# Kernel optimization log

Measured on AMD Instinct MI355X. Metric: run time of the kernel, lower is better.

## Reference

```python
import jax, jax.numpy as jnp
import numpy as np


def setup_inputs() -> dict:
    B, D, H, O = 16, 128, 2048, 4
    W = O * H + O  # 8196 flattened last-layer params
    ks = jax.random.split(jax.random.key(0), 6)
    return {
        "x": jax.random.normal(ks[0], (B, D), dtype=jnp.float32),
        "W1": jax.random.normal(ks[1], (H, D), dtype=jnp.float32) * 0.05,
        "b1": jax.random.normal(ks[2], (H,), dtype=jnp.float32) * 0.01,
        "W2": jax.random.normal(ks[3], (O, H), dtype=jnp.float32) * 0.02,
        "b2": jax.random.normal(ks[4], (O,), dtype=jnp.float32) * 0.01,
        "inv_covariance": jax.random.normal(ks[5], (W, W), dtype=jnp.float32) * 0.01,
    }


def reference(x, W1, b1, W2, b2, inv_covariance):
    # Wrapped model: MLP with ReLU; uncertainty layer = last Linear(H->O).
    O, H = W2.shape
    h = jax.nn.relu(x @ W1.T + b1)          # [B, H] penultimate activations
    predictions = h @ W2.T + b2             # [B, O]

    # Jacobian of each output element w.r.t. flattened last-layer params
    # (weight then bias), matching torch's per-output autograd.grad loop but
    # vectorized: vmap over batch of jacrev over the parameter vector.
    p0 = jnp.concatenate([W2.reshape(-1), b2])  # [W]

    def head(p, h_b):
        w2 = p[: O * H].reshape(O, H)
        b = p[O * H :]
        return h_b @ w2.T + b               # [O]

    J = jax.vmap(lambda h_b: jax.jacrev(head)(p0, h_b))(h)  # [B, O, W]

    # uncertainty = diag of per-(b,o) quadratic form J Sigma^{-1} J^T
    uncertainty = jnp.einsum('bow,wv,bov->bo', J, inv_covariance, J)
    return predictions, uncertainty
```

## Files before the change

kernel.cpp:

```cpp
#include <hip/hip_runtime.h>

#define BB 16
#define DD 128
#define HH 2048
#define OO 4
#define WTOT 8196
#define OHH 8192
#define KC 32
#define NQUAD 512
#define NCROSS 32


__global__ __launch_bounds__(256) void k_prep(const float* __restrict__ x,
                                              const float* __restrict__ W1,
                                              const float* __restrict__ b1,
                                              float* __restrict__ hT) {
    __shared__ float xs[DD * BB];
    int tid = threadIdx.x;
    for (int i = tid; i < DD * BB; i += 256) {
        int b = i & 15, d = i >> 4;
        xs[i] = x[b * DD + d];
    }
    __syncthreads();
    int b = tid & 15;
    int j = blockIdx.x * 16 + (tid >> 4);
    const float4* W1v = (const float4*)(W1 + (size_t)j * DD);
    float acc = 0.0f;
#pragma unroll
    for (int dd = 0; dd < DD / 4; ++dd) {
        float4 w = W1v[dd];
        acc = fmaf(xs[(dd * 4 + 0) * 16 + b], w.x, acc);
        acc = fmaf(xs[(dd * 4 + 1) * 16 + b], w.y, acc);
        acc = fmaf(xs[(dd * 4 + 2) * 16 + b], w.z, acc);
        acc = fmaf(xs[(dd * 4 + 3) * 16 + b], w.w, acc);
    }
    acc += b1[j];
    hT[j * 16 + b] = acc > 0.0f ? acc : 0.0f;
}

__global__ __launch_bounds__(256) void k_main(const float* __restrict__ C,
                                              const float* __restrict__ hT,
                                              const float* __restrict__ W2,
                                              float* __restrict__ qpart,
                                              float* __restrict__ xu,
                                              float* __restrict__ xp) {
    int bid = blockIdx.x;
    int tid = threadIdx.x;
    __shared__ float sh[KC * 16];
    __shared__ float red[4 * 16];

    if (bid < NQUAD) {
        int o  = bid & 3;
        int ct = (bid >> 2) & 1;
        int kc = bid >> 3;
        if (tid < KC * 16 / 4)
            ((float4*)sh)[tid] = ((const float4*)(hT + (size_t)kc * KC * 16))[tid];
        __syncthreads();

        int base = o * HH;
        const float4* Cp = (const float4*)(C + (size_t)(base + kc * KC) * WTOT
                                             + base + ct * 1024) + tid;
        float acc[16][4];
#pragma unroll
        for (int b = 0; b < 16; ++b)
#pragma unroll
            for (int c = 0; c < 4; ++c) acc[b][c] = 0.0f;

#pragma unroll 4
        for (int k = 0; k < KC; ++k) {
            float4 c4 = Cp[(size_t)k * (WTOT / 4)];
#pragma unroll
            for (int b = 0; b < 16; ++b) {
                float hb = sh[k * 16 + b];
                acc[b][0] = fmaf(hb, c4.x, acc[b][0]);
                acc[b][1] = fmaf(hb, c4.y, acc[b][1]);
                acc[b][2] = fmaf(hb, c4.z, acc[b][2]);
                acc[b][3] = fmaf(hb, c4.w, acc[b][3]);
            }
        }

        int col0 = ct * 1024 + 4 * tid;
        float v[16];
#pragma unroll
        for (int b = 0; b < 16; ++b) v[b] = 0.0f;
#pragma unroll
        for (int c = 0; c < 4; ++c) {
            const float* hc = hT + (size_t)(col0 + c) * 16;
#pragma unroll
            for (int b = 0; b < 16; ++b)
                v[b] = fmaf(acc[b][c], hc[b], v[b]);
        }

#pragma unroll
        for (int b = 0; b < 16; ++b) {
            float s = v[b];
#pragma unroll
            for (int off = 32; off > 0; off >>= 1)
                s += __shfl_down(s, off, 64);
            v[b] = s;
        }
        int lane = tid & 63, wv = tid >> 6;
        if (lane == 0) {
#pragma unroll
            for (int b = 0; b < 16; ++b) red[wv * 16 + b] = v[b];
        }
        __syncthreads();
        if (tid < 16)
            qpart[bid * 16 + tid] = red[tid] + red[16 + tid] + red[32 + tid] + red[48 + tid];
    } else {
        int cb = bid - NQUAD;
        int o  = cb & 3;
        int kb = cb >> 2;
        int b = tid >> 4, g = tid & 15;
        int base = o * HH;
        float a12 = 0.0f, ap = 0.0f;
#pragma unroll 4
        for (int i = 0; i < 16; ++i) {
            int k = kb * 256 + i * 16 + g;
            float hv = hT[k * 16 + b];
            float c1 = C[(size_t)(base + k) * WTOT + OHH + o];
            float c2 = C[(size_t)(OHH + o) * WTOT + base + k];
            float w2 = W2[o * HH + k];
            a12 = fmaf(hv, c1 + c2, a12);
            ap  = fmaf(hv, w2, ap);
        }
#pragma unroll
        for (int off = 8; off > 0; off >>= 1) {
            a12 += __shfl_down(a12, off, 16);
            ap  += __shfl_down(ap, off, 16);
        }
        if (g == 0) {
            xu[cb * 16 + b] = a12;
            xp[cb * 16 + b] = ap;
        }
    }
}

__global__ void k_final(const float* __restrict__ C,
                        const float* __restrict__ qpart,
                        const float* __restrict__ xu,
                        const float* __restrict__ xp,
                        const float* __restrict__ b2,
                        float* __restrict__ out) {
    int i = threadIdx.x;
    int b = i >> 2, o = i & 3;
    float u = 0.0f, p = 0.0f;
    for (int q = o; q < NQUAD; q += 4) u += qpart[q * 16 + b];
    for (int c = o; c < NCROSS; c += 4) {
        u += xu[c * 16 + b];
        p += xp[c * 16 + b];
    }
    out[i] = p + b2[o];
    out[64 + i] = u + C[(size_t)(OHH + o) * WTOT + OHH + o];
}

extern "C" void kernel_launch(void* const* d_in, const int* in_sizes, int n_in,
                              void* d_out, int out_size, void* d_ws, size_t ws_size,
                              hipStream_t stream) {
    const float* x  = (const float*)d_in[0];
    const float* W1 = (const float*)d_in[1];
    const float* b1 = (const float*)d_in[2];
    const float* W2 = (const float*)d_in[3];
    const float* b2 = (const float*)d_in[4];
    const float* C  = (const float*)d_in[5];
    float* out = (float*)d_out;

    float* hT    = (float*)d_ws;
    float* qpart = hT + HH * BB;
    float* xu    = qpart + NQUAD * 16;
    float* xp    = xu + NCROSS * 16;

    hipLaunchKernelGGL(k_prep,  dim3(HH / 16),        dim3(256), 0, stream, x, W1, b1, hT);
    hipLaunchKernelGGL(k_main,  dim3(NQUAD + NCROSS), dim3(256), 0, stream, C, hT, W2, qpart, xu, xp);
    hipLaunchKernelGGL(k_final, dim3(1),              dim3(64),  0, stream, C, qpart, xu, xp, b2, out);
}
```

Measured before the change: 362.2 us.

## Double-buffer C tiles into LDS via async global_load_lds in main kernel

The quadratic-form blocks now stream C rows into LDS using the async global-to-LDS load builtin, in groups of 8 rows with double buffering. Each group's compute overlaps with the prefetch of the next group, replacing direct per-thread global loads in the inner loop. Launch bounds now request 2 blocks per CU. The final reduction kernel is also widened from 64 to 256 threads with a shared-memory combine. The change adds 64KB of LDS per block, which limits occupancy, and adds a barrier per group.

```diff
diff --git a/kernel.cpp b/kernel.cpp
--- a/kernel.cpp
+++ b/kernel.cpp
@@ -7,8 +7,13 @@
 #define WTOT 8196
 #define OHH 8192
 #define KC 32
+#define GG 8
+#define NG (KC / GG)
 #define NQUAD 512
 #define NCROSS 32
+
+typedef const __attribute__((address_space(1))) float glob_f;
+typedef __attribute__((address_space(3))) float lds_f;
 
 
 __global__ __launch_bounds__(256) void k_prep(const float* __restrict__ x,
@@ -38,59 +43,80 @@
     hT[j * 16 + b] = acc > 0.0f ? acc : 0.0f;
 }
 
-__global__ __launch_bounds__(256) void k_main(const float* __restrict__ C,
-                                              const float* __restrict__ hT,
-                                              const float* __restrict__ W2,
-                                              float* __restrict__ qpart,
-                                              float* __restrict__ xu,
-                                              float* __restrict__ xp) {
+__global__ __launch_bounds__(256, 2) void k_main(const float* __restrict__ C,
+                                                 const float* __restrict__ hT,
+                                                 const float* __restrict__ W2,
+                                                 float* __restrict__ qpart,
+                                                 float* __restrict__ xu,
+                                                 float* __restrict__ xp) {
+    __shared__ float bufs[2 * GG * 1024];
+    __shared__ float sh[KC * BB];
+    __shared__ float red[4 * BB];
     int bid = blockIdx.x;
     int tid = threadIdx.x;
-    __shared__ float sh[KC * 16];
-    __shared__ float red[4 * 16];
 
     if (bid < NQUAD) {
         int o  = bid & 3;
         int ct = (bid >> 2) & 1;
         int kc = bid >> 3;
-        if (tid < KC * 16 / 4)
-            ((float4*)sh)[tid] = ((const float4*)(hT + (size_t)kc * KC * 16))[tid];
-        __syncthreads();
-
         int base = o * HH;
-        const float4* Cp = (const float4*)(C + (size_t)(base + kc * KC) * WTOT
-                                             + base + ct * 1024) + tid;
+        int row0 = base + kc * KC;
+        int col0 = base + ct * 1024;
+
+        if (tid < KC * BB / 4)
+            ((float4*)sh)[tid] = ((const float4*)(hT + (size_t)kc * KC * BB))[tid];
+
+        glob_f* gsrc = (glob_f*)(C + (size_t)row0 * WTOT + col0 + tid * 4);
+        lds_f*  ld0  = (lds_f*)(bufs) + tid * 4;
+
+#pragma unroll
+        for (int r = 0; r < GG; ++r)
+            __builtin_amdgcn_global_load_lds(gsrc + (size_t)r * WTOT,
+                                             ld0 + r * 1024, 16, 0, 0);
+
         float acc[16][4];
 #pragma unroll
         for (int b = 0; b < 16; ++b)
 #pragma unroll
             for (int c = 0; c < 4; ++c) acc[b][c] = 0.0f;
 
-#pragma unroll 4
-        for (int k = 0; k < KC; ++k) {
-            float4 c4 = Cp[(size_t)k * (WTOT / 4)];
-#pragma unroll
-            for (int b = 0; b < 16; ++b) {
-                float hb = sh[k * 16 + b];
-                acc[b][0] = fmaf(hb, c4.x, acc[b][0]);
-                acc[b][1] = fmaf(hb, c4.y, acc[b][1]);
-                acc[b][2] = fmaf(hb, c4.z, acc[b][2]);
-                acc[b][3] = fmaf(hb, c4.w, acc[b][3]);
+        for (int g = 0; g < NG; ++g) {
+            __syncthreads();
+            if (g + 1 < NG) {
+                glob_f* gs = gsrc + (size_t)(g + 1) * GG * WTOT;
+                lds_f*  ls = (lds_f*)(bufs) + ((g + 1) & 1) * (GG * 1024) + tid * 4;
+#pragma unroll
+                for (int r = 0; r < GG; ++r)
+                    __builtin_amdgcn_global_load_lds(gs + (size_t)r * WTOT,
+                                                     ls + r * 1024, 16, 0, 0);
             }
-        }
-
-        int col0 = ct * 1024 + 4 * tid;
+            const float* bp = bufs + (g & 1) * (GG * 1024);
+#pragma unroll
+            for (int k = 0; k < GG; ++k) {
+                float4 c4 = ((const float4*)(bp + k * 1024))[tid];
+                int kk = g * GG + k;
+#pragma unroll
+                for (int b = 0; b < 16; ++b) {
+                    float hb = sh[kk * 16 + b];
+                    acc[b][0] = fmaf(hb, c4.x, acc[b][0]);
+                    acc[b][1] = fmaf(hb, c4.y, acc[b][1]);
+                    acc[b][2] = fmaf(hb, c4.z, acc[b][2]);
+                    acc[b][3] = fmaf(hb, c4.w, acc[b][3]);
+                }
+            }
+        }
+
+        int col0l = ct * 1024 + 4 * tid;
         float v[16];
 #pragma unroll
         for (int b = 0; b < 16; ++b) v[b] = 0.0f;
 #pragma unroll
         for (int c = 0; c < 4; ++c) {
-            const float* hc = hT + (size_t)(col0 + c) * 16;
+            const float* hc = hT + (size_t)(col0l + c) * 16;
 #pragma unroll
             for (int b = 0; b < 16; ++b)
                 v[b] = fmaf(acc[b][c], hc[b], v[b]);
         }
-
 #pragma unroll
         for (int b = 0; b < 16; ++b) {
             float s = v[b];
@@ -136,22 +162,35 @@
     }
 }
 
-__global__ void k_final(const float* __restrict__ C,
-                        const float* __restrict__ qpart,
-                        const float* __restrict__ xu,
-                        const float* __restrict__ xp,
-                        const float* __restrict__ b2,
-                        float* __restrict__ out) {
-    int i = threadIdx.x;
+__global__ __launch_bounds__(256) void k_final(const float* __restrict__ C,
+                                               const float* __restrict__ qpart,
+                                               const float* __restrict__ xu,
+                                               const float* __restrict__ xp,
+                                               const float* __restrict__ b2,
+                                               float* __restrict__ out) {
+    __shared__ float s[256];
+    int tid = threadIdx.x;
+    int i = tid & 63;
+    int p = tid >> 6;
     int b = i >> 2, o = i & 3;
-    float u = 0.0f, p = 0.0f;
-    for (int q = o; q < NQUAD; q += 4) u += qpart[q * 16 + b];
-    for (int c = o; c < NCROSS; c += 4) {
-        u += xu[c * 16 + b];
-        p += xp[c * 16 + b];
-    }
-    out[i] = p + b2[o];
-    out[64 + i] = u + C[(size_t)(OHH + o) * WTOT + OHH + o];
+    float u = 0.0f;
+#pragma unroll 4
+    for (int m = p; m < NQUAD / 4; m += 4)
+        u += qpart[(o + 4 * m) * 16 + b];
+    if (p == 0) {
+#pragma unroll
+        for (int c = o; c < NCROSS; c += 4) u += xu[c * 16 + b];
+    }
+    s[tid] = u;
+    __syncthreads();
+    if (tid < 64) {
+        float uu = s[tid] + s[64 + tid] + s[128 + tid] + s[192 + tid];
+        float pp = 0.0f;
+#pragma unroll
+        for (int c = o; c < NCROSS; c += 4) pp += xp[c * 16 + b];
+        out[i] = pp + b2[o];
+        out[64 + i] = uu + C[(size_t)(OHH + o) * WTOT + OHH + o];
+    }
 }
 
 extern "C" void kernel_launch(void* const* d_in, const int* in_sizes, int n_in,
@@ -172,5 +211,5 @@
 
     hipLaunchKernelGGL(k_prep,  dim3(HH / 16),        dim3(256), 0, stream, x, W1, b1, hT);
     hipLaunchKernelGGL(k_main,  dim3(NQUAD + NCROSS), dim3(256), 0, stream, C, hT, W2, qpart, xu, xp);
-    hipLaunchKernelGGL(k_final, dim3(1),              dim3(64),  0, stream, C, qpart, xu, xp, b2, out);
-}
+    hipLaunchKernelGGL(k_final, dim3(1),              dim3(256), 0, stream, C, qpart, xu, xp, b2, out);
+}
```

Result: faster. 330.0 us (-8.9%).
